# Kernel optimization log

Hardware: AMD Instinct MI355X
Metric: run time of the kernel (lower is better)

Reference implementation:

```python
import jax, jax.numpy as jnp
import numpy as np

D_MODEL = 256; N_HEADS = 8; N_LEVELS = 4; N_POINTS = 4; D_FFN = 1024
BS = 8; NQ = 100; NKPT = 17
LEVEL_SHAPES = [(160, 160), (80, 80), (40, 40), (20, 20)]  # (H, W) per level
LEN_V = sum(h * w for h, w in LEVEL_SHAPES)  # 34000


def layer_norm(x, g, b, eps=1e-5):
    m = x.mean(-1, keepdims=True)
    v = ((x - m) ** 2).mean(-1, keepdims=True)
    return (x - m) * jax.lax.rsqrt(v + eps) * g + b


def mha(q, k, v, Wqkv, bqkv, Wo, bo):
    # torch nn.MultiheadAttention, batch_first, eval mode (no dropout)
    d = q.shape[-1]; dh = d // N_HEADS
    def proj(x, W, b):
        return (x @ W.T + b).reshape(*x.shape[:-1], N_HEADS, dh)
    qp = proj(q, Wqkv[:d], bqkv[:d])
    kp = proj(k, Wqkv[d:2 * d], bqkv[d:2 * d])
    vp = proj(v, Wqkv[2 * d:], bqkv[2 * d:])
    att = jnp.einsum('bqhd,bkhd->bhqk', qp, kp) / jnp.sqrt(jnp.asarray(dh, q.dtype))
    att = jax.nn.softmax(att, -1)
    out = jnp.einsum('bhqk,bkhd->bqhd', att, vp).reshape(q.shape)
    return out @ Wo.T + bo


def bilinear_sample(val, loc, h, w):
    # val: (B, H, h*w, Dh); loc: (B, Lq, H, P, 2) normalized to [0,1]
    # matches F.grid_sample(align_corners=False, padding_mode='zeros') on grid 2*loc-1
    B, Lq, H, P, _ = loc.shape
    px = loc[..., 0] * w - 0.5
    py = loc[..., 1] * h - 0.5
    x0f = jnp.floor(px); y0f = jnp.floor(py)
    lx = px - x0f; ly = py - y0f
    x0 = x0f.astype(jnp.int32); y0 = y0f.astype(jnp.int32)
    out = jnp.zeros((B, H, Lq, P, val.shape[-1]), val.dtype)
    for dx, dy, wt in ((0, 0, (1 - lx) * (1 - ly)), (1, 0, lx * (1 - ly)),
                       (0, 1, (1 - lx) * ly), (1, 1, lx * ly)):
        xi = x0 + dx; yi = y0 + dy
        valid = ((xi >= 0) & (xi < w) & (yi >= 0) & (yi < h)).astype(val.dtype)
        idx = jnp.clip(yi, 0, h - 1) * w + jnp.clip(xi, 0, w - 1)  # (B,Lq,H,P)
        idx = idx.transpose(0, 2, 1, 3).reshape(B, H, Lq * P)
        g = jnp.take_along_axis(val, idx[..., None], axis=2).reshape(B, H, Lq, P, -1)
        out = out + g * (wt * valid).transpose(0, 2, 1, 3)[..., None]
    return out  # (B, H, Lq, P, Dh)


def ms_deform_attn(query, ref_points, memory, off_W, off_b, aw_W, aw_b,
                   val_W, val_b, outp_W, outp_b):
    B, Lq, _ = query.shape
    dh = D_MODEL // N_HEADS
    value = (memory @ val_W.T + val_b).reshape(B, LEN_V, N_HEADS, dh)
    off = (query @ off_W.T + off_b).reshape(B, Lq, N_HEADS, N_LEVELS, N_POINTS, 2)
    aw = (query @ aw_W.T + aw_b).reshape(B, Lq, N_HEADS, N_LEVELS * N_POINTS)
    aw = jax.nn.softmax(aw, -1).reshape(B, Lq, N_HEADS, N_LEVELS, N_POINTS)
    normalizer = jnp.array([[w, h] for h, w in LEVEL_SHAPES], dtype=query.dtype)  # (L,2) as (W,H)
    loc = ref_points[:, :, None, :, None, :] + off / normalizer[None, None, None, :, None, :]
    out = jnp.zeros((B, Lq, N_HEADS, dh), query.dtype)
    start = 0
    for l, (h, w) in enumerate(LEVEL_SHAPES):
        vl = value[:, start:start + h * w].transpose(0, 2, 1, 3)  # (B,H,hw,Dh)
        s = bilinear_sample(vl, loc[:, :, :, l], h, w)            # (B,H,Lq,P,Dh)
        out = out + jnp.einsum('bhqpd,bqhp->bqhd', s, aw[:, :, :, l])
        start += h * w
    return out.reshape(B, Lq, D_MODEL) @ outp_W.T + outp_b


def setup_inputs() -> dict:
    key = jax.random.key(0)
    ks = iter(jax.random.split(key, 40))
    d = D_MODEL
    def w(shape, s=0.02):
        return jax.random.normal(next(ks), shape, jnp.float32) * s
    inp = {
        'tgt_pose': jax.random.normal(next(ks), (BS, NQ, NKPT, d), jnp.float32),
        'tgt_pose_query_pos': jax.random.normal(next(ks), (BS, NQ, NKPT, d), jnp.float32),
        'tgt_pose_reference_points': jax.random.uniform(next(ks), (BS, NQ * NKPT, N_LEVELS, 2), jnp.float32),
        'memory': jax.random.normal(next(ks), (BS, LEN_V, d), jnp.float32),
        'win_Wqkv': w((3 * d, d)), 'win_bqkv': jnp.zeros((3 * d,), jnp.float32),
        'win_Wo': w((d, d)), 'win_bo': jnp.zeros((d,), jnp.float32),
        'win_ng': jnp.ones((d,), jnp.float32), 'win_nb': jnp.zeros((d,), jnp.float32),
        'acr_Wqkv': w((3 * d, d)), 'acr_bqkv': jnp.zeros((3 * d,), jnp.float32),
        'acr_Wo': w((d, d)), 'acr_bo': jnp.zeros((d,), jnp.float32),
        'acr_ng': jnp.ones((d,), jnp.float32), 'acr_nb': jnp.zeros((d,), jnp.float32),
        'off_W': w((N_HEADS * N_LEVELS * N_POINTS * 2, d)),
        'off_b': jax.random.uniform(next(ks), (N_HEADS * N_LEVELS * N_POINTS * 2,), jnp.float32, -1.0, 1.0),
        'aw_W': w((N_HEADS * N_LEVELS * N_POINTS, d)), 'aw_b': jnp.zeros((N_HEADS * N_LEVELS * N_POINTS,), jnp.float32),
        'val_W': w((d, d)), 'val_b': jnp.zeros((d,), jnp.float32),
        'outp_W': w((d, d)), 'outp_b': jnp.zeros((d,), jnp.float32),
        'gate_W': w((2 * d, 2 * d)), 'gate_b': jnp.zeros((2 * d,), jnp.float32),
        'gate_ng': jnp.ones((d,), jnp.float32), 'gate_nb': jnp.zeros((d,), jnp.float32),
        'ffn_W1': w((D_FFN, d)), 'ffn_b1': jnp.zeros((D_FFN,), jnp.float32),
        'ffn_W2': w((d, D_FFN)), 'ffn_b2': jnp.zeros((d,), jnp.float32),
        'n2_g': jnp.ones((d,), jnp.float32), 'n2_b': jnp.zeros((d,), jnp.float32),
        'memory_spatial_shapes': jnp.array(LEVEL_SHAPES, jnp.int32),
    }
    return inp


def reference(tgt_pose, tgt_pose_query_pos, tgt_pose_reference_points, memory,
              win_Wqkv, win_bqkv, win_Wo, win_bo, win_ng, win_nb,
              acr_Wqkv, acr_bqkv, acr_Wo, acr_bo, acr_ng, acr_nb,
              off_W, off_b, aw_W, aw_b, val_W, val_b, outp_W, outp_b,
              gate_W, gate_b, gate_ng, gate_nb,
              ffn_W1, ffn_b1, ffn_W2, ffn_b2, n2_g, n2_b,
              memory_spatial_shapes):
    bs, nq, K, d = tgt_pose.shape
    # with_pos_embed mutates tgt_pose in place in the torch code -> residual includes pos
    tgt = tgt_pose + tgt_pose_query_pos
    # within-attention over keypoints of each query
    x = tgt.reshape(bs * nq, K, d)
    t2 = mha(x, x, x, win_Wqkv, win_bqkv, win_Wo, win_bo).reshape(bs, nq, K, d)
    tgt = layer_norm(tgt + t2, win_ng, win_nb)
    # across-attention over queries for each keypoint
    xk = tgt.transpose(0, 2, 1, 3).reshape(bs * K, nq, d)
    t2 = mha(xk, xk, xk, acr_Wqkv, acr_bqkv, acr_Wo, acr_bo)
    tgt = layer_norm(xk + t2, acr_ng, acr_nb).reshape(bs, K, nq, d).transpose(0, 2, 1, 3)
    # second in-place pos add before deformable cross-attn (also feeds gateway)
    tgt_q = tgt + tgt_pose_query_pos
    t2 = ms_deform_attn(tgt_q.reshape(bs, nq * K, d), tgt_pose_reference_points, memory,
                        off_W, off_b, aw_W, aw_b, val_W, val_b, outp_W, outp_b)
    t2 = t2.reshape(bs, nq, K, d)
    # Gate
    g = jax.nn.sigmoid(jnp.concatenate([tgt_q, t2], -1) @ gate_W.T + gate_b)
    g1, g2 = jnp.split(g, 2, -1)
    tgt = layer_norm(g1 * tgt_q + g2 * t2, gate_ng, gate_nb)
    # FFN
    h = jax.nn.relu(tgt @ ffn_W1.T + ffn_b1)
    tgt = tgt + h @ ffn_W2.T + ffn_b2
    tgt = layer_norm(jnp.clip(tgt, -65504.0, 65504.0), n2_g, n2_b)
    return tgt
```

## Files before the change

### kernel.cpp

```cpp
#include <hip/hip_runtime.h>
#include <hip/hip_bf16.h>

#define NH 8
#define BS_ 8
#define NQ_ 100
#define NK_ 17
#define LQ 1700
#define T_TOK 13600
#define LEN_VV 34000

typedef __attribute__((ext_vector_type(8))) short short8v;
typedef __attribute__((ext_vector_type(8))) __bf16 bf16x8;
typedef __attribute__((ext_vector_type(4))) float f32x4;

__device__ __forceinline__ float wave_sum(float v){
#pragma unroll
  for (int m = 32; m; m >>= 1) v += __shfl_xor(v, m, 64);
  return v;
}
__device__ __forceinline__ short f2bf(float f){
  __hip_bfloat16 h = __float2bfloat16(f);
  return *reinterpret_cast<short*>(&h);
}
__device__ __forceinline__ float bf2f(short s){
  return __uint_as_float(((uint)(unsigned short)s) << 16);
}

__global__ __launch_bounds__(256) void add_k(const float* __restrict__ a,
                                             const float* __restrict__ b,
                                             float* __restrict__ o, int n4){
  int i = blockIdx.x * 256 + threadIdx.x;
  if (i >= n4) return;
  float4 x = ((const float4*)a)[i];
  float4 y = ((const float4*)b)[i];
  float4 r; r.x = x.x + y.x; r.y = x.y + y.y; r.z = x.z + y.z; r.w = x.w + y.w;
  ((float4*)o)[i] = r;
}

template<int EPI, int OUTB>
__global__ __launch_bounds__(256) void mgemm_k(const float* __restrict__ A,
                                               const float* __restrict__ W,
                                               const float* __restrict__ bias,
                                               float* __restrict__ Cf,
                                               __hip_bfloat16* __restrict__ Cb,
                                               int M, int N, int K){
  __shared__ short sh[OUTB ? 128 * 136 : 128 * 128];
  short* As = sh;
  short* Ws = sh + 128 * 64;
  const int tid = threadIdx.x;
  const int bm = blockIdx.y * 128, bn = blockIdx.x * 128;
  const int wave = tid >> 6, lane = tid & 63;
  const int wm = (wave >> 1) * 64, wn = (wave & 1) * 64;
  const int s = tid & 7;
  const int row0 = tid >> 3;
  f32x4 acc[4][4] = {};
  const int lrow = lane & 15, lk = lane >> 4;

  float4 ra[8], rw[8];
#pragma unroll
  for (int i = 0; i < 4; i++){
    int row = row0 + i * 32;
    int gr = bm + row;
    float4 z = make_float4(0.f, 0.f, 0.f, 0.f);
    if (gr < M){
      const float* p = A + (size_t)gr * K + s * 8;
      ra[2 * i] = ((const float4*)p)[0]; ra[2 * i + 1] = ((const float4*)p)[1];
    } else { ra[2 * i] = z; ra[2 * i + 1] = z; }
    const float* q = W + (size_t)(bn + row) * K + s * 8;
    rw[2 * i] = ((const float4*)q)[0]; rw[2 * i + 1] = ((const float4*)q)[1];
  }

  for (int k0 = 0; k0 < K; k0 += 64){
#pragma unroll
    for (int i = 0; i < 4; i++){
      int row = row0 + i * 32;
      int sw = ((s ^ (row & 7)) << 3) + row * 64;
      float4 a0 = ra[2 * i], a1 = ra[2 * i + 1];
      short8v v;
      v[0]=f2bf(a0.x); v[1]=f2bf(a0.y); v[2]=f2bf(a0.z); v[3]=f2bf(a0.w);
      v[4]=f2bf(a1.x); v[5]=f2bf(a1.y); v[6]=f2bf(a1.z); v[7]=f2bf(a1.w);
      *(short8v*)&As[sw] = v;
      a0 = rw[2 * i]; a1 = rw[2 * i + 1];
      short8v u;
      u[0]=f2bf(a0.x); u[1]=f2bf(a0.y); u[2]=f2bf(a0.z); u[3]=f2bf(a0.w);
      u[4]=f2bf(a1.x); u[5]=f2bf(a1.y); u[6]=f2bf(a1.z); u[7]=f2bf(a1.w);
      *(short8v*)&Ws[sw] = u;
    }
    __syncthreads();
    if (k0 + 64 < K){
#pragma unroll
      for (int i = 0; i < 4; i++){
        int row = row0 + i * 32;
        int gr = bm + row;
        float4 z = make_float4(0.f, 0.f, 0.f, 0.f);
        if (gr < M){
          const float* p = A + (size_t)gr * K + k0 + 64 + s * 8;
          ra[2 * i] = ((const float4*)p)[0]; ra[2 * i + 1] = ((const float4*)p)[1];
        } else { ra[2 * i] = z; ra[2 * i + 1] = z; }
        const float* q = W + (size_t)(bn + row) * K + k0 + 64 + s * 8;
        rw[2 * i] = ((const float4*)q)[0]; rw[2 * i + 1] = ((const float4*)q)[1];
      }
    }
#pragma unroll
    for (int ks = 0; ks < 2; ks++){
      short8v af[4], bw[4];
      int slot = ks * 4 + lk;
#pragma unroll
      for (int m = 0; m < 4; m++){
        int r = wm + m * 16 + lrow;
        af[m] = *(const short8v*)&As[r * 64 + ((slot ^ (r & 7)) << 3)];
      }
#pragma unroll
      for (int n = 0; n < 4; n++){
        int r = wn + n * 16 + lrow;
        bw[n] = *(const short8v*)&Ws[r * 64 + ((slot ^ (r & 7)) << 3)];
      }
#pragma unroll
      for (int m = 0; m < 4; m++)
#pragma unroll
        for (int n = 0; n < 4; n++)
          acc[m][n] = __builtin_amdgcn_mfma_f32_16x16x32_bf16(
              __builtin_bit_cast(bf16x8, af[m]),
              __builtin_bit_cast(bf16x8, bw[n]), acc[m][n], 0, 0, 0);
    }
    __syncthreads();
  }
  if (OUTB){
    const int STR = 136;
#pragma unroll
    for (int n = 0; n < 4; n++){
      int col = wn + n * 16 + lrow;
      float bsv = bias[bn + col];
#pragma unroll
      for (int m = 0; m < 4; m++){
#pragma unroll
        for (int i = 0; i < 4; i++){
          int row = wm + m * 16 + lk * 4 + i;
          float c = acc[m][n][i] + bsv;
          if (EPI == 1) c = fmaxf(c, 0.f);
          if (EPI == 2) c = 1.f / (1.f + expf(-c));
          sh[row * STR + col] = f2bf(c);
        }
      }
    }
    __syncthreads();
#pragma unroll
    for (int it = 0; it < 8; it++){
      int r = it * 16 + (tid >> 4);
      int chunk = tid & 15;
      if (bm + r < M){
        uint4 v = *(const uint4*)((const char*)sh + r * 272 + chunk * 16);
        *(uint4*)((char*)Cb + ((size_t)(bm + r) * N + bn) * 2 + chunk * 16) = v;
      }
    }
  } else {
#pragma unroll
    for (int n = 0; n < 4; n++){
      int col = bn + wn + n * 16 + lrow;
      float bsv = bias[col];
#pragma unroll
      for (int m = 0; m < 4; m++){
#pragma unroll
        for (int i = 0; i < 4; i++){
          int row = bm + wm + m * 16 + lk * 4 + i;
          if (row >= M) continue;
          float c = acc[m][n][i] + bsv;
          if (EPI == 1) c = fmaxf(c, 0.f);
          if (EPI == 2) c = 1.f / (1.f + expf(-c));
          Cf[(size_t)row * N + col] = c;
        }
      }
    }
  }
}

template<int EPI, int OUTB, int INB, int DUALA>
__global__ __launch_bounds__(256) void g64_k(const void* __restrict__ Av,
                                             const void* __restrict__ A1v,
                                             const float* __restrict__ W0,
                                             const float* __restrict__ W1,
                                             int NSPLIT,
                                             const float* __restrict__ bias0,
                                             const float* __restrict__ bias1,
                                             float* __restrict__ Cf,
                                             __hip_bfloat16* __restrict__ Cb,
                                             int M, int N, int K, int sA){
  __shared__ short sh64[2 * 64 * 64];
  short* As = sh64;
  short* Ws = sh64 + 64 * 64;
  const int tid = threadIdx.x;
  const int bn = blockIdx.x * 64, bm = blockIdx.y * 64;
  const int wave = tid >> 6, lane = tid & 63;
  const int wm = (wave >> 1) * 32, wn = (wave & 1) * 32;
  const int s = tid & 7, row0 = tid >> 3;
  const int lrow = lane & 15, lk = lane >> 4;
  f32x4 acc[2][2] = {};

  for (int k0 = 0; k0 < K; k0 += 64){
#pragma unroll
    for (int i = 0; i < 2; i++){
      int row = row0 + i * 32;
      int sw = ((s ^ (row & 7)) << 3) + row * 64;
      short8v v = {};
      int gr = bm + row;
      if (gr < M){
        if (INB){
          v = *(const short8v*)((const short*)Av + (size_t)gr * sA + k0 + s * 8);
        } else {
          const float* Ap;
          if (DUALA) Ap = (k0 < 256) ? (const float*)Av + (size_t)gr * 256 + k0
                                     : (const float*)A1v + (size_t)gr * 256 + (k0 - 256);
          else Ap = (const float*)Av + (size_t)gr * sA + k0;
          float4 a0 = ((const float4*)(Ap + s * 8))[0];
          float4 a1 = ((const float4*)(Ap + s * 8))[1];
          v[0]=f2bf(a0.x); v[1]=f2bf(a0.y); v[2]=f2bf(a0.z); v[3]=f2bf(a0.w);
          v[4]=f2bf(a1.x); v[5]=f2bf(a1.y); v[6]=f2bf(a1.z); v[7]=f2bf(a1.w);
        }
      }
      *(short8v*)&As[sw] = v;
      int wr = bn + row;
      const float* Wp = (wr < NSPLIT) ? W0 + (size_t)wr * K + k0
                                      : W1 + (size_t)(wr - NSPLIT) * K + k0;
      float4 b0 = ((const float4*)(Wp + s * 8))[0];
      float4 b1 = ((const float4*)(Wp + s * 8))[1];
      short8v u;
      u[0]=f2bf(b0.x); u[1]=f2bf(b0.y); u[2]=f2bf(b0.z); u[3]=f2bf(b0.w);
      u[4]=f2bf(b1.x); u[5]=f2bf(b1.y); u[6]=f2bf(b1.z); u[7]=f2bf(b1.w);
      *(short8v*)&Ws[sw] = u;
    }
    __syncthreads();
#pragma unroll
    for (int ks = 0; ks < 2; ks++){
      int slot = ks * 4 + lk;
      short8v af[2], bw[2];
#pragma unroll
      for (int m = 0; m < 2; m++){
        int r = wm + m * 16 + lrow;
        af[m] = *(const short8v*)&As[r * 64 + ((slot ^ (r & 7)) << 3)];
      }
#pragma unroll
      for (int n = 0; n < 2; n++){
        int r = wn + n * 16 + lrow;
        bw[n] = *(const short8v*)&Ws[r * 64 + ((slot ^ (r & 7)) << 3)];
      }
#pragma unroll
      for (int m = 0; m < 2; m++)
#pragma unroll
        for (int n = 0; n < 2; n++)
          acc[m][n] = __builtin_amdgcn_mfma_f32_16x16x32_bf16(
              __builtin_bit_cast(bf16x8, af[m]),
              __builtin_bit_cast(bf16x8, bw[n]), acc[m][n], 0, 0, 0);
    }
    __syncthreads();
  }
  if (OUTB){
    const int STR = 72;
#pragma unroll
    for (int n = 0; n < 2; n++){
      int col = wn + n * 16 + lrow;
      int gc = bn + col;
      float bsv = (gc < NSPLIT) ? bias0[gc] : bias1[gc - NSPLIT];
#pragma unroll
      for (int m = 0; m < 2; m++){
#pragma unroll
        for (int i = 0; i < 4; i++){
          int row = wm + m * 16 + lk * 4 + i;
          float c = acc[m][n][i] + bsv;
          if (EPI == 1) c = fmaxf(c, 0.f);
          if (EPI == 2) c = 1.f / (1.f + expf(-c));
          sh64[row * STR + col] = f2bf(c);
        }
      }
    }
    __syncthreads();
#pragma unroll
    for (int it = 0; it < 2; it++){
      int r = it * 32 + (tid >> 3);
      int chunk = tid & 7;
      if (bm + r < M){
        uint4 v = *(const uint4*)((const char*)sh64 + r * 144 + chunk * 16);
        *(uint4*)((char*)Cb + ((size_t)(bm + r) * N + bn) * 2 + chunk * 16) = v;
      }
    }
  } else {
#pragma unroll
    for (int n = 0; n < 2; n++){
      int gc = bn + wn + n * 16 + lrow;
      float bsv = (gc < NSPLIT) ? bias0[gc] : bias1[gc - NSPLIT];
#pragma unroll
      for (int m = 0; m < 2; m++){
#pragma unroll
        for (int i = 0; i < 4; i++){
          int row = bm + wm + m * 16 + lk * 4 + i;
          if (row >= M) continue;
          float c = acc[m][n][i] + bsv;
          if (EPI == 1) c = fmaxf(c, 0.f);
          if (EPI == 2) c = 1.f / (1.f + expf(-c));
          Cf[(size_t)row * N + gc] = c;
        }
      }
    }
  }
}

template<int TP>
__global__ __launch_bounds__(256) void mha_mfma_k(const short* __restrict__ qkv,
                                                  __hip_bfloat16* __restrict__ out, int S){
  constexpr int MT = TP / 16;
  constexpr int KSTEPS = (TP + 31) / 32;
  constexpr int KS32 = KSTEPS * 32;
  constexpr int VSTRB = (KS32 == 128) ? 256 : 128;
  __shared__ short QK[2][TP][64];
  __shared__ short Vt[2][32][VSTRB / 2];
  __shared__ float Sc[2][16][128];
  __shared__ float rinv[2][16];

  const int tid = threadIdx.x;
  const int bid = blockIdx.x;
  const int batch = bid >> 2, hp = bid & 3;
  const int wave = tid >> 6, lane = tid & 63;
  const int hh = wave >> 1, wsub = wave & 1;
  const int lrow = lane & 15, lk = lane >> 4;
  const float scale = 0.17677669529663687f;
  const size_t qbase = (size_t)batch * S * 768;

  for (int idx = tid; idx < 2 * TP * 4; idx += 256){
    int h2 = idx >= TP * 4;
    int rem = idx - h2 * TP * 4;
    int j = rem >> 2, s = rem & 3;
    int h = hp * 2 + h2;
    short8v qv = {}, kv = {};
    if (j < S){
      const short* p = qkv + qbase + (size_t)j * 768 + h * 32 + s * 8;
      qv = *(const short8v*)p;
      kv = *(const short8v*)(p + 256);
    }
    *(short8v*)&QK[h2][j][(s ^ (j & 7)) << 3] = qv;
    *(short8v*)&QK[h2][j][((s + 4) ^ (j & 7)) << 3] = kv;
  }
  for (int idx = tid; idx < 2 * KS32 * 4; idx += 256){
    int h2 = idx >= KS32 * 4;
    int rem = idx - h2 * KS32 * 4;
    int j = rem >> 2, e8 = rem & 3;
    int h = hp * 2 + h2;
    short8v v = {};
    if (j < S) v = *(const short8v*)(qkv + qbase + (size_t)j * 768 + h * 32 + 512 + e8 * 8);
#pragma unroll
    for (int c = 0; c < 8; c++){
      int e = e8 * 8 + c;
      char* pb = (char*)&Vt[h2][0][0] + e * VSTRB + (((j >> 3) ^ (e & 7)) << 4) + ((j & 7) << 1);
      *(short*)pb = v[c];
    }
  }
  __syncthreads();

  for (int mt = 0; mt < MT; mt++){
    for (int nt = wsub; nt < MT; nt += 2){
      int ar = mt * 16 + lrow;
      short8v aq = *(const short8v*)&QK[hh][ar][(lk ^ (ar & 7)) << 3];
      int br = nt * 16 + lrow;
      short8v bk = *(const short8v*)&QK[hh][br][((lk + 4) ^ (br & 7)) << 3];
      f32x4 z = {};
      f32x4 d = __builtin_amdgcn_mfma_f32_16x16x32_bf16(
          __builtin_bit_cast(bf16x8, aq), __builtin_bit_cast(bf16x8, bk), z, 0, 0, 0);
#pragma unroll
      for (int i = 0; i < 4; i++){
        int rr = lk * 4 + i;
        int c = nt * 16 + lrow;
        Sc[hh][rr][(((c >> 2) ^ (rr & 7)) << 2) + (c & 3)] = d[i] * scale;
      }
    }
    __syncthreads();
    if (wsub == 0){
      int rr = lane >> 2, p = lane & 3;
      int grow = mt * 16 + rr;
      int Seff = (grow < S) ? S : 0;
      float mx = -1e30f;
#pragma unroll
      for (int m = 0; m < KSTEPS; m++){
        int j = p + 4 * m;
#pragma unroll
        for (int half = 0; half < 2; half++){
          int ls = 2 * j + half;
          float4 v = *(const float4*)&Sc[hh][rr][(ls ^ (rr & 7)) << 2];
          int c0 = ls * 4;
          mx = fmaxf(mx, (c0 + 0 < Seff) ? v.x : -1e30f);
          mx = fmaxf(mx, (c0 + 1 < Seff) ? v.y : -1e30f);
          mx = fmaxf(mx, (c0 + 2 < Seff) ? v.z : -1e30f);
          mx = fmaxf(mx, (c0 + 3 < Seff) ? v.w : -1e30f);
        }
      }
      mx = fmaxf(mx, __shfl_xor(mx, 1, 64));
      mx = fmaxf(mx, __shfl_xor(mx, 2, 64));
      float sum = 0.f;
#pragma unroll
      for (int m = 0; m < KSTEPS; m++){
        int j = p + 4 * m;
        float ev[8];
#pragma unroll
        for (int half = 0; half < 2; half++){
          int ls = 2 * j + half;
          float4 v = *(const float4*)&Sc[hh][rr][(ls ^ (rr & 7)) << 2];
          int c0 = ls * 4;
          ev[half * 4 + 0] = (c0 + 0 < Seff) ? __expf(v.x - mx) : 0.f;
          ev[half * 4 + 1] = (c0 + 1 < Seff) ? __expf(v.y - mx) : 0.f;
          ev[half * 4 + 2] = (c0 + 2 < Seff) ? __expf(v.z - mx) : 0.f;
          ev[half * 4 + 3] = (c0 + 3 < Seff) ? __expf(v.w - mx) : 0.f;
        }
        short8v pb;
#pragma unroll
        for (int q2 = 0; q2 < 8; q2++){ pb[q2] = f2bf(ev[q2]); sum += ev[q2]; }
        *(short8v*)((char*)&Sc[hh][rr][0] + ((j ^ (rr & 7)) << 4)) = pb;
      }
      sum += __shfl_xor(sum, 1, 64);
      sum += __shfl_xor(sum, 2, 64);
      if (p == 0) rinv[hh][rr] = (sum > 0.f) ? 1.f / sum : 0.f;
    }
    __syncthreads();
    {
      int nt2 = wsub;
      f32x4 acc = {};
#pragma unroll
      for (int ks = 0; ks < KSTEPS; ks++){
        int slot = ks * 4 + lk;
        short8v ap = *(const short8v*)((const char*)&Sc[hh][lrow][0] + ((slot ^ (lrow & 7)) << 4));
        int e = nt2 * 16 + lrow;
        short8v bv = *(const short8v*)((const char*)&Vt[hh][0][0] + e * VSTRB + ((slot ^ (e & 7)) << 4));
        acc = __builtin_amdgcn_mfma_f32_16x16x32_bf16(
            __builtin_bit_cast(bf16x8, ap), __builtin_bit_cast(bf16x8, bv), acc, 0, 0, 0);
      }
      int h = hp * 2 + hh;
#pragma unroll
      for (int i = 0; i < 4; i++){
        int row = mt * 16 + lk * 4 + i;
        if (row < S){
          float rv = rinv[hh][lk * 4 + i];
          out[((size_t)batch * S + row) * 256 + h * 32 + nt2 * 16 + lrow] =
              __float2bfloat16(acc[i] * rv);
        }
      }
    }
    __syncthreads();
  }
}

template<int MODE>
__global__ __launch_bounds__(64) void ln_k(const float* __restrict__ a,
                                           const float* __restrict__ b,
                                           const float* __restrict__ g,
                                           const float* __restrict__ be,
                                           float* __restrict__ out,
                                           const float* __restrict__ qp){
  int r = blockIdx.x;
  int lane = threadIdx.x;
  float4 xa = *(const float4*)(a + (size_t)r * 256 + lane * 4);
  float4 xb = *(const float4*)(b + (size_t)r * 256 + lane * 4);
  float x[4] = { xa.x + xb.x, xa.y + xb.y, xa.z + xb.z, xa.w + xb.w };
  if (MODE == 2){
#pragma unroll
    for (int i = 0; i < 4; i++) x[i] = fminf(fmaxf(x[i], -65504.f), 65504.f);
  }
  float s = x[0] + x[1] + x[2] + x[3];
  s = wave_sum(s);
  float mean = s * (1.f / 256.f);
  float sq = 0.f;
#pragma unroll
  for (int i = 0; i < 4; i++){ float d = x[i] - mean; sq += d * d; }
  float var = wave_sum(sq) * (1.f / 256.f);
  float rstd = rsqrtf(var + 1e-5f);
  float4 gg = *(const float4*)(g + lane * 4);
  float4 bb = *(const float4*)(be + lane * 4);
  size_t orow = r;
  if (MODE == 3){
    int bi = r / LQ; int rem = r % LQ; int kk = rem / NQ_; int q = rem % NQ_;
    orow = (size_t)bi * LQ + q * NK_ + kk;
  }
  if (MODE == 4){
    int bi = r / LQ; int rem = r % LQ; int q = rem / NK_; int kk = rem % NK_;
    orow = (size_t)bi * LQ + kk * NQ_ + q;
  }
  float4 o;
  o.x = (x[0] - mean) * rstd * gg.x + bb.x;
  o.y = (x[1] - mean) * rstd * gg.y + bb.y;
  o.z = (x[2] - mean) * rstd * gg.z + bb.z;
  o.w = (x[3] - mean) * rstd * gg.w + bb.w;
  if (MODE == 3){
    float4 qv = *(const float4*)(qp + orow * 256 + lane * 4);
    o.x += qv.x; o.y += qv.y; o.z += qv.z; o.w += qv.w;
  }
  *(float4*)(out + orow * 256 + lane * 4) = o;
}

__global__ __launch_bounds__(64) void gate_ln_k(const short* __restrict__ G,
                                                const float* __restrict__ aq,
                                                const float* __restrict__ t2,
                                                const float* __restrict__ g,
                                                const float* __restrict__ be,
                                                float* __restrict__ out){
  int r = blockIdx.x;
  int lane = threadIdx.x;
  const short* gp = G + (size_t)r * 512 + lane * 4;
  float g1v[4], g2v[4];
#pragma unroll
  for (int i = 0; i < 4; i++){ g1v[i] = bf2f(gp[i]); g2v[i] = bf2f(gp[256 + i]); }
  float4 xa = *(const float4*)(aq + (size_t)r * 256 + lane * 4);
  float4 xt = *(const float4*)(t2 + (size_t)r * 256 + lane * 4);
  float x[4] = { g1v[0] * xa.x + g2v[0] * xt.x, g1v[1] * xa.y + g2v[1] * xt.y,
                 g1v[2] * xa.z + g2v[2] * xt.z, g1v[3] * xa.w + g2v[3] * xt.w };
  float s = x[0] + x[1] + x[2] + x[3];
  s = wave_sum(s);
  float mean = s * (1.f / 256.f);
  float sq = 0.f;
#pragma unroll
  for (int i = 0; i < 4; i++){ float d = x[i] - mean; sq += d * d; }
  float var = wave_sum(sq) * (1.f / 256.f);
  float rstd = rsqrtf(var + 1e-5f);
  float4 gg = *(const float4*)(g + lane * 4);
  float4 bb = *(const float4*)(be + lane * 4);
  float4 o;
  o.x = (x[0] - mean) * rstd * gg.x + bb.x;
  o.y = (x[1] - mean) * rstd * gg.y + bb.y;
  o.z = (x[2] - mean) * rstd * gg.z + bb.z;
  o.w = (x[3] - mean) * rstd * gg.w + bb.w;
  *(float4*)(out + (size_t)r * 256 + lane * 4) = o;
}

__global__ __launch_bounds__(256) void deform_k(const __hip_bfloat16* __restrict__ val,
                                                const float* __restrict__ offaw,
                                                const float* __restrict__ ref,
                                                unsigned int* __restrict__ outb){
  __shared__ uint2 meta[32][16][4];
  const int tid = threadIdx.x;
  const int t0 = blockIdx.x * 4;
  {
    int g = tid >> 3;
    int pair = tid & 7;
    int lt = g >> 3, h = g & 7;
    int t = t0 + lt;
    int b = t / LQ;
    int p0 = pair * 2;
    int l = p0 >> 2;
    const int starts[4] = {0, 25600, 32000, 33600};
    const int HS[4] = {160, 80, 40, 20};
    int w = HS[l];
    const float* ap = offaw + (size_t)t * 384 + 256 + h * 16;
    float a0 = ap[p0];
    float a1 = ap[p0 + 1];
    float mx = fmaxf(a0, a1);
#pragma unroll
    for (int m = 1; m <= 4; m <<= 1) mx = fmaxf(mx, __shfl_xor(mx, m, 64));
    float e0 = expf(a0 - mx), e1 = expf(a1 - mx);
    float s = e0 + e1;
#pragma unroll
    for (int m = 1; m <= 4; m <<= 1) s += __shfl_xor(s, m, 64);
    float inv = 1.f / s;
    float rx = ref[((size_t)t * 4 + l) * 2 + 0];
    float ry = ref[((size_t)t * 4 + l) * 2 + 1];
    float4 ov = *(const float4*)(offaw + (size_t)t * 384 + h * 32 + l * 8 + p0 * 2);
    int vbase = (b * LEN_VV + starts[l]) * 128 + h * 16;
#pragma unroll
    for (int pp = 0; pp < 2; pp++){
      float wgt = (pp ? e1 : e0) * inv;
      float px = rx * w + (pp ? ov.z : ov.x) - 0.5f;
      float py = ry * w + (pp ? ov.w : ov.y) - 0.5f;
      float x0f = floorf(px), y0f = floorf(py);
      float lx = px - x0f, ly = py - y0f;
      int x0 = (int)x0f, y0 = (int)y0f;
#pragma unroll
      for (int c = 0; c < 4; c++){
        int dx = c & 1, dy = c >> 1;
        int xi = x0 + dx, yi = y0 + dy;
        bool ok = (xi >= 0) & (xi < w) & (yi >= 0) & (yi < w);
        float cw = ok ? wgt * (dx ? lx : 1.f - lx) * (dy ? ly : 1.f - ly) : 0.f;
        uint idx = ok ? (uint)(vbase + (yi * w + xi) * 128) : 0u;
        uint2 m2; m2.x = idx; m2.y = __float_as_uint(cw);
        meta[g][p0 + pp][c] = m2;
      }
    }
  }
  __syncthreads();
  const uint* V2 = (const uint*)val;
  int sg = tid >> 4, lane = tid & 15;
#pragma unroll
  for (int it = 0; it < 2; it++){
    int g = it * 16 + sg;
    int lt = g >> 3, h = g & 7;
    int t = t0 + lt;
    float ax = 0.f, ay = 0.f;
#pragma unroll 4
    for (int c = 0; c < 64; c++){
      uint2 mw = meta[g][c >> 2][c & 3];
      float wv = __uint_as_float(mw.y);
      uint v = V2[(size_t)mw.x + lane];
      float lo = __uint_as_float(v << 16);
      float hi = __uint_as_float(v & 0xffff0000u);
      ax += wv * lo;
      ay += wv * hi;
    }
    uint u = ((uint)(unsigned short)f2bf(ay) << 16) | (uint)(unsigned short)f2bf(ax);
    outb[((size_t)t * 256 + h * 32) / 2 + lane] = u;
  }
}

extern "C" void kernel_launch(void* const* d_in, const int* in_sizes, int n_in,
                              void* d_out, int out_size, void* d_ws, size_t ws_size,
                              hipStream_t stream){
  const float* tgt_pose = (const float*)d_in[0];
  const float* qpos     = (const float*)d_in[1];
  const float* refp     = (const float*)d_in[2];
  const float* memory   = (const float*)d_in[3];
  const float* win_Wqkv = (const float*)d_in[4];
  const float* win_bqkv = (const float*)d_in[5];
  const float* win_Wo   = (const float*)d_in[6];
  const float* win_bo   = (const float*)d_in[7];
  const float* win_ng   = (const float*)d_in[8];
  const float* win_nb   = (const float*)d_in[9];
  const float* acr_Wqkv = (const float*)d_in[10];
  const float* acr_bqkv = (const float*)d_in[11];
  const float* acr_Wo   = (const float*)d_in[12];
  const float* acr_bo   = (const float*)d_in[13];
  const float* acr_ng   = (const float*)d_in[14];
  const float* acr_nb   = (const float*)d_in[15];
  const float* off_W    = (const float*)d_in[16];
  const float* off_b    = (const float*)d_in[17];
  const float* aw_W     = (const float*)d_in[18];
  const float* aw_b     = (const float*)d_in[19];
  const float* val_W    = (const float*)d_in[20];
  const float* val_b    = (const float*)d_in[21];
  const float* outp_W   = (const float*)d_in[22];
  const float* outp_b   = (const float*)d_in[23];
  const float* gate_W   = (const float*)d_in[24];
  const float* gate_b   = (const float*)d_in[25];
  const float* gate_ng  = (const float*)d_in[26];
  const float* gate_nb  = (const float*)d_in[27];
  const float* ffn_W1   = (const float*)d_in[28];
  const float* ffn_b1   = (const float*)d_in[29];
  const float* ffn_W2   = (const float*)d_in[30];
  const float* ffn_b2   = (const float*)d_in[31];
  const float* n2_g     = (const float*)d_in[32];
  const float* n2_b     = (const float*)d_in[33];

  float* out = (float*)d_out;
  char* ws = (char*)d_ws;
  const size_t TB = (size_t)T_TOK * 256 * 4;
  float* B0 = (float*)(ws);
  float* B1 = (float*)(ws + TB);
  float* B2 = (float*)(ws + 2 * TB);
  float* B3 = (float*)(ws + 3 * TB);
  char* p = ws + 4 * TB;
  short* Qb = (short*)p;                 p += (size_t)T_TOK * 768 * 2;
  short* ABF = (short*)p;                p += (size_t)T_TOK * 256 * 2;
  float* OFFAW = (float*)p;              p += (size_t)T_TOK * 384 * 4;
  short* Gb = (short*)p;                 p += (size_t)T_TOK * 512 * 2;
  char* Vregion = p;
  __hip_bfloat16* V = (__hip_bfloat16*)Vregion;
  short* FF = (short*)Vregion;

  const int n4 = T_TOK * 64;
  const int GM128 = (T_TOK + 127) / 128;
  const int GM64  = (T_TOK + 63) / 64;
  const int BIG = 1 << 30;

  add_k<<<(n4 + 255) / 256, 256, 0, stream>>>(tgt_pose, qpos, B0, n4);
  mgemm_k<0,1><<<dim3(6, GM128), 256, 0, stream>>>(B0, win_Wqkv, win_bqkv, nullptr, (__hip_bfloat16*)Qb, T_TOK, 768, 256);
  mha_mfma_k<32><<<800 * 4, 256, 0, stream>>>(Qb, (__hip_bfloat16*)ABF, 17);
  g64_k<0,0,1,0><<<dim3(4, GM64), 256, 0, stream>>>(ABF, nullptr, win_Wo, win_Wo, BIG, win_bo, win_bo, B2, nullptr, T_TOK, 256, 256, 256);
  ln_k<4><<<T_TOK, 64, 0, stream>>>(B0, B2, win_ng, win_nb, B1, nullptr);
  mgemm_k<0,1><<<dim3(6, GM128), 256, 0, stream>>>(B1, acr_Wqkv, acr_bqkv, nullptr, (__hip_bfloat16*)Qb, T_TOK, 768, 256);
  mha_mfma_k<112><<<136 * 4, 256, 0, stream>>>(Qb, (__hip_bfloat16*)ABF, 100);
  g64_k<0,0,1,0><<<dim3(4, GM64), 256, 0, stream>>>(ABF, nullptr, acr_Wo, acr_Wo, BIG, acr_bo, acr_bo, B2, nullptr, T_TOK, 256, 256, 256);
  ln_k<3><<<T_TOK, 64, 0, stream>>>(B1, B2, acr_ng, acr_nb, B0, qpos);
  mgemm_k<0,1><<<dim3(2, 2125), 256, 0, stream>>>(memory, val_W, val_b, nullptr, V, BS_ * LEN_VV, 256, 256);
  g64_k<0,0,0,0><<<dim3(6, GM64), 256, 0, stream>>>(B0, nullptr, off_W, aw_W, 256, off_b, aw_b, OFFAW, nullptr, T_TOK, 384, 256, 256);
  deform_k<<<T_TOK / 4, 256, 0, stream>>>(V, OFFAW, refp, (unsigned int*)ABF);
  g64_k<0,0,1,0><<<dim3(4, GM64), 256, 0, stream>>>(ABF, nullptr, outp_W, outp_W, BIG, outp_b, outp_b, B3, nullptr, T_TOK, 256, 256, 256);
  g64_k<2,1,0,1><<<dim3(8, GM64), 256, 0, stream>>>(B0, B3, gate_W, gate_W, BIG, gate_b, gate_b, nullptr, (__hip_bfloat16*)Gb, T_TOK, 512, 512, 256);
  gate_ln_k<<<T_TOK, 64, 0, stream>>>(Gb, B0, B3, gate_ng, gate_nb, B2);
  mgemm_k<1,1><<<dim3(8, GM128), 256, 0, stream>>>(B2, ffn_W1, ffn_b1, nullptr, (__hip_bfloat16*)FF, T_TOK, 1024, 256);
  g64_k<0,0,1,0><<<dim3(4, GM64), 256, 0, stream>>>(FF, nullptr, ffn_W2, ffn_W2, BIG, ffn_b2, ffn_b2, B1, nullptr, T_TOK, 256, 1024, 1024);
  ln_k<2><<<T_TOK, 64, 0, stream>>>(B2, B1, n2_g, n2_b, out, nullptr);
}
```

Measured before the change: 465.4 us.

## Fuse pos-add into QKV GEMM, split MHA blocks, swizzle value GEMM grid

Removes the standalone add kernel by summing tgt and query_pos inside the QKV GEMM loads, and re-adds query_pos in the layernorm instead. Folds the FFN residual into the second FFN GEMM epilogue so the final layernorm reads one tensor. Splits the across-query attention over two blocks per head pair for more parallelism. Also remaps the value-projection GEMM grid to a 1D layout with an XCD-aware swizzle and launches it first. The cost is more loads inside the GEMM and duplicated Q/K/V staging in the split attention blocks.

Result: no change. 472.6 us (+1.6%).

```diff
diff --git a/kernel.cpp b/kernel.cpp
--- a/kernel.cpp
+++ b/kernel.cpp
@@ -26,29 +26,27 @@
   return __uint_as_float(((uint)(unsigned short)s) << 16);
 }
 
-__global__ __launch_bounds__(256) void add_k(const float* __restrict__ a,
-                                             const float* __restrict__ b,
-                                             float* __restrict__ o, int n4){
-  int i = blockIdx.x * 256 + threadIdx.x;
-  if (i >= n4) return;
-  float4 x = ((const float4*)a)[i];
-  float4 y = ((const float4*)b)[i];
-  float4 r; r.x = x.x + y.x; r.y = x.y + y.y; r.z = x.z + y.z; r.w = x.w + y.w;
-  ((float4*)o)[i] = r;
-}
-
-template<int EPI, int OUTB>
+template<int EPI, int ADDA, int SWZ>
 __global__ __launch_bounds__(256) void mgemm_k(const float* __restrict__ A,
+                                               const float* __restrict__ A2,
                                                const float* __restrict__ W,
                                                const float* __restrict__ bias,
-                                               float* __restrict__ Cf,
                                                __hip_bfloat16* __restrict__ Cb,
-                                               int M, int N, int K){
-  __shared__ short sh[OUTB ? 128 * 136 : 128 * 128];
+                                               int M, int N, int K, int nbx){
+  __shared__ short sh[128 * 136];
   short* As = sh;
   short* Ws = sh + 128 * 64;
+  int j;
+  if (SWZ){
+    int total = gridDim.x;
+    int q = total >> 3, r = total & 7;
+    int x = blockIdx.x & 7, k = blockIdx.x >> 3;
+    j = (x < r) ? x * (q + 1) + k : r * (q + 1) + (x - r) * q + k;
+  } else {
+    j = blockIdx.x;
+  }
   const int tid = threadIdx.x;
-  const int bm = blockIdx.y * 128, bn = blockIdx.x * 128;
+  const int bm = (j / nbx) * 128, bn = (j % nbx) * 128;
   const int wave = tid >> 6, lane = tid & 63;
   const int wm = (wave >> 1) * 64, wn = (wave & 1) * 64;
   const int s = tid & 7;
@@ -64,7 +62,14 @@
     float4 z = make_float4(0.f, 0.f, 0.f, 0.f);
     if (gr < M){
       const float* p = A + (size_t)gr * K + s * 8;
-      ra[2 * i] = ((const float4*)p)[0]; ra[2 * i + 1] = ((const float4*)p)[1];
+      float4 x0 = ((const float4*)p)[0], x1 = ((const float4*)p)[1];
+      if (ADDA){
+        const float* q2 = A2 + (size_t)gr * K + s * 8;
+        float4 y0 = ((const float4*)q2)[0], y1 = ((const float4*)q2)[1];
+        x0.x+=y0.x; x0.y+=y0.y; x0.z+=y0.z; x0.w+=y0.w;
+        x1.x+=y1.x; x1.y+=y1.y; x1.z+=y1.z; x1.w+=y1.w;
+      }
+      ra[2 * i] = x0; ra[2 * i + 1] = x1;
     } else { ra[2 * i] = z; ra[2 * i + 1] = z; }
     const float* q = W + (size_t)(bn + row) * K + s * 8;
     rw[2 * i] = ((const float4*)q)[0]; rw[2 * i + 1] = ((const float4*)q)[1];
@@ -95,7 +100,14 @@
         float4 z = make_float4(0.f, 0.f, 0.f, 0.f);
         if (gr < M){
           const float* p = A + (size_t)gr * K + k0 + 64 + s * 8;
-          ra[2 * i] = ((const float4*)p)[0]; ra[2 * i + 1] = ((const float4*)p)[1];
+          float4 x0 = ((const float4*)p)[0], x1 = ((const float4*)p)[1];
+          if (ADDA){
+            const float* q2 = A2 + (size_t)gr * K + k0 + 64 + s * 8;
+            float4 y0 = ((const float4*)q2)[0], y1 = ((const float4*)q2)[1];
+            x0.x+=y0.x; x0.y+=y0.y; x0.z+=y0.z; x0.w+=y0.w;
+            x1.x+=y1.x; x1.y+=y1.y; x1.z+=y1.z; x1.w+=y1.w;
+          }
+          ra[2 * i] = x0; ra[2 * i + 1] = x1;
         } else { ra[2 * i] = z; ra[2 * i + 1] = z; }
         const float* q = W + (size_t)(bn + row) * K + k0 + 64 + s * 8;
         rw[2 * i] = ((const float4*)q)[0]; rw[2 * i + 1] = ((const float4*)q)[1];
@@ -125,51 +137,30 @@
     }
     __syncthreads();
   }
-  if (OUTB){
-    const int STR = 136;
-#pragma unroll
-    for (int n = 0; n < 4; n++){
-      int col = wn + n * 16 + lrow;
-      float bsv = bias[bn + col];
-#pragma unroll
-      for (int m = 0; m < 4; m++){
-#pragma unroll
-        for (int i = 0; i < 4; i++){
-          int row = wm + m * 16 + lk * 4 + i;
-          float c = acc[m][n][i] + bsv;
-          if (EPI == 1) c = fmaxf(c, 0.f);
-          if (EPI == 2) c = 1.f / (1.f + expf(-c));
-          sh[row * STR + col] = f2bf(c);
-        }
-      }
-    }
-    __syncthreads();
-#pragma unroll
-    for (int it = 0; it < 8; it++){
-      int r = it * 16 + (tid >> 4);
-      int chunk = tid & 15;
-      if (bm + r < M){
-        uint4 v = *(const uint4*)((const char*)sh + r * 272 + chunk * 16);
-        *(uint4*)((char*)Cb + ((size_t)(bm + r) * N + bn) * 2 + chunk * 16) = v;
-      }
-    }
-  } else {
-#pragma unroll
-    for (int n = 0; n < 4; n++){
-      int col = bn + wn + n * 16 + lrow;
-      float bsv = bias[col];
-#pragma unroll
-      for (int m = 0; m < 4; m++){
-#pragma unroll
-        for (int i = 0; i < 4; i++){
-          int row = bm + wm + m * 16 + lk * 4 + i;
-          if (row >= M) continue;
-          float c = acc[m][n][i] + bsv;
-          if (EPI == 1) c = fmaxf(c, 0.f);
-          if (EPI == 2) c = 1.f / (1.f + expf(-c));
-          Cf[(size_t)row * N + col] = c;
-        }
-      }
+  const int STR = 136;
+#pragma unroll
+  for (int n = 0; n < 4; n++){
+    int col = wn + n * 16 + lrow;
+    float bsv = bias[bn + col];
+#pragma unroll
+    for (int m = 0; m < 4; m++){
+#pragma unroll
+      for (int i = 0; i < 4; i++){
+        int row = wm + m * 16 + lk * 4 + i;
+        float c = acc[m][n][i] + bsv;
+        if (EPI == 1) c = fmaxf(c, 0.f);
+        sh[row * STR + col] = f2bf(c);
+      }
+    }
+  }
+  __syncthreads();
+#pragma unroll
+  for (int it = 0; it < 8; it++){
+    int r = it * 16 + (tid >> 4);
+    int chunk = tid & 15;
+    if (bm + r < M){
+      uint4 v = *(const uint4*)((const char*)sh + r * 272 + chunk * 16);
+      *(uint4*)((char*)Cb + ((size_t)(bm + r) * N + bn) * 2 + chunk * 16) = v;
     }
   }
 }
@@ -182,6 +173,7 @@
                                              int NSPLIT,
                                              const float* __restrict__ bias0,
                                              const float* __restrict__ bias1,
+                                             const float* __restrict__ RES,
                                              float* __restrict__ Cf,
                                              __hip_bfloat16* __restrict__ Cb,
                                              int M, int N, int K, int sA){
@@ -296,6 +288,7 @@
           float c = acc[m][n][i] + bsv;
           if (EPI == 1) c = fmaxf(c, 0.f);
           if (EPI == 2) c = 1.f / (1.f + expf(-c));
+          if (EPI == 3) c += RES[(size_t)row * N + gc];
           Cf[(size_t)row * N + gc] = c;
         }
       }
@@ -303,13 +296,14 @@
   }
 }
 
-template<int TP>
+template<int TP, int NSPL>
 __global__ __launch_bounds__(256) void mha_mfma_k(const short* __restrict__ qkv,
                                                   __hip_bfloat16* __restrict__ out, int S){
   constexpr int MT = TP / 16;
   constexpr int KSTEPS = (TP + 31) / 32;
   constexpr int KS32 = KSTEPS * 32;
   constexpr int VSTRB = (KS32 == 128) ? 256 : 128;
+  constexpr int CH = (MT + NSPL - 1) / NSPL;
   __shared__ short QK[2][TP][64];
   __shared__ short Vt[2][32][VSTRB / 2];
   __shared__ float Sc[2][16][128];
@@ -317,7 +311,12 @@
 
   const int tid = threadIdx.x;
   const int bid = blockIdx.x;
-  const int batch = bid >> 2, hp = bid & 3;
+  const int batch = bid / (4 * NSPL);
+  const int rem = bid % (4 * NSPL);
+  const int hp = rem / NSPL;
+  const int half = rem % NSPL;
+  const int mtlo = half * CH;
+  const int mthi = (mtlo + CH < MT) ? (mtlo + CH) : MT;
   const int wave = tid >> 6, lane = tid & 63;
   const int hh = wave >> 1, wsub = wave & 1;
   const int lrow = lane & 15, lk = lane >> 4;
@@ -326,8 +325,8 @@
 
   for (int idx = tid; idx < 2 * TP * 4; idx += 256){
     int h2 = idx >= TP * 4;
-    int rem = idx - h2 * TP * 4;
-    int j = rem >> 2, s = rem & 3;
+    int rm = idx - h2 * TP * 4;
+    int j = rm >> 2, s = rm & 3;
     int h = hp * 2 + h2;
     short8v qv = {}, kv = {};
     if (j < S){
@@ -340,8 +339,8 @@
   }
   for (int idx = tid; idx < 2 * KS32 * 4; idx += 256){
     int h2 = idx >= KS32 * 4;
-    int rem = idx - h2 * KS32 * 4;
-    int j = rem >> 2, e8 = rem & 3;
+    int rm = idx - h2 * KS32 * 4;
+    int j = rm >> 2, e8 = rm & 3;
     int h = hp * 2 + h2;
     short8v v = {};
     if (j < S) v = *(const short8v*)(qkv + qbase + (size_t)j * 768 + h * 32 + 512 + e8 * 8);
@@ -354,7 +353,7 @@
   }
   __syncthreads();
 
-  for (int mt = 0; mt < MT; mt++){
+  for (int mt = mtlo; mt < mthi; mt++){
     for (int nt = wsub; nt < MT; nt += 2){
       int ar = mt * 16 + lrow;
       short8v aq = *(const short8v*)&QK[hh][ar][(lk ^ (ar & 7)) << 3];
@@ -380,8 +379,8 @@
       for (int m = 0; m < KSTEPS; m++){
         int j = p + 4 * m;
 #pragma unroll
-        for (int half = 0; half < 2; half++){
-          int ls = 2 * j + half;
+        for (int hf = 0; hf < 2; hf++){
+          int ls = 2 * j + hf;
           float4 v = *(const float4*)&Sc[hh][rr][(ls ^ (rr & 7)) << 2];
           int c0 = ls * 4;
           mx = fmaxf(mx, (c0 + 0 < Seff) ? v.x : -1e30f);
@@ -398,14 +397,14 @@
         int j = p + 4 * m;
         float ev[8];
 #pragma unroll
-        for (int half = 0; half < 2; half++){
-          int ls = 2 * j + half;
+        for (int hf = 0; hf < 2; hf++){
+          int ls = 2 * j + hf;
           float4 v = *(const float4*)&Sc[hh][rr][(ls ^ (rr & 7)) << 2];
           int c0 = ls * 4;
-          ev[half * 4 + 0] = (c0 + 0 < Seff) ? __expf(v.x - mx) : 0.f;
-          ev[half * 4 + 1] = (c0 + 1 < Seff) ? __expf(v.y - mx) : 0.f;
-          ev[half * 4 + 2] = (c0 + 2 < Seff) ? __expf(v.z - mx) : 0.f;
-          ev[half * 4 + 3] = (c0 + 3 < Seff) ? __expf(v.w - mx) : 0.f;
+          ev[hf * 4 + 0] = (c0 + 0 < Seff) ? __expf(v.x - mx) : 0.f;
+          ev[hf * 4 + 1] = (c0 + 1 < Seff) ? __expf(v.y - mx) : 0.f;
+          ev[hf * 4 + 2] = (c0 + 2 < Seff) ? __expf(v.z - mx) : 0.f;
+          ev[hf * 4 + 3] = (c0 + 3 < Seff) ? __expf(v.w - mx) : 0.f;
         }
         short8v pb;
 #pragma unroll
@@ -450,13 +449,21 @@
                                            const float* __restrict__ g,
                                            const float* __restrict__ be,
                                            float* __restrict__ out,
-                                           const float* __restrict__ qp){
+                                           const float* __restrict__ qpre,
+                                           const float* __restrict__ qpost){
   int r = blockIdx.x;
   int lane = threadIdx.x;
   float4 xa = *(const float4*)(a + (size_t)r * 256 + lane * 4);
-  float4 xb = *(const float4*)(b + (size_t)r * 256 + lane * 4);
-  float x[4] = { xa.x + xb.x, xa.y + xb.y, xa.z + xb.z, xa.w + xb.w };
-  if (MODE == 2){
+  float x[4] = { xa.x, xa.y, xa.z, xa.w };
+  if (MODE != 5){
+    float4 xb = *(const float4*)(b + (size_t)r * 256 + lane * 4);
+    x[0] += xb.x; x[1] += xb.y; x[2] += xb.z; x[3] += xb.w;
+  }
+  if (MODE == 4){
+    float4 xq = *(const float4*)(qpre + (size_t)r * 256 + lane * 4);
+    x[0] += xq.x; x[1] += xq.y; x[2] += xq.z; x[3] += xq.w;
+  }
+  if (MODE == 5){
 #pragma unroll
     for (int i = 0; i < 4; i++) x[i] = fminf(fmaxf(x[i], -65504.f), 65504.f);
   }
@@ -485,7 +492,7 @@
   o.z = (x[2] - mean) * rstd * gg.z + bb.z;
   o.w = (x[3] - mean) * rstd * gg.w + bb.w;
   if (MODE == 3){
-    float4 qv = *(const float4*)(qp + orow * 256 + lane * 4);
+    float4 qv = *(const float4*)(qpost + orow * 256 + lane * 4);
     o.x += qv.x; o.y += qv.y; o.z += qv.z; o.w += qv.w;
   }
   *(float4*)(out + orow * 256 + lane * 4) = o;
@@ -567,7 +574,7 @@
       float lx = px - x0f, ly = py - y0f;
       int x0 = (int)x0f, y0 = (int)y0f;
 #pragma unroll
-      for (int c = 0; c < 4; c++){
+    for (int c = 0; c < 4; c++){
         int dx = c & 1, dy = c >> 1;
         int xi = x0 + dx, yi = y0 + dy;
         bool ok = (xi >= 0) & (xi < w) & (yi >= 0) & (yi < w);
@@ -656,27 +663,25 @@
   __hip_bfloat16* V = (__hip_bfloat16*)Vregion;
   short* FF = (short*)Vregion;
 
-  const int n4 = T_TOK * 64;
   const int GM128 = (T_TOK + 127) / 128;
   const int GM64  = (T_TOK + 63) / 64;
   const int BIG = 1 << 30;
 
-  add_k<<<(n4 + 255) / 256, 256, 0, stream>>>(tgt_pose, qpos, B0, n4);
-  mgemm_k<0,1><<<dim3(6, GM128), 256, 0, stream>>>(B0, win_Wqkv, win_bqkv, nullptr, (__hip_bfloat16*)Qb, T_TOK, 768, 256);
-  mha_mfma_k<32><<<800 * 4, 256, 0, stream>>>(Qb, (__hip_bfloat16*)ABF, 17);
-  g64_k<0,0,1,0><<<dim3(4, GM64), 256, 0, stream>>>(ABF, nullptr, win_Wo, win_Wo, BIG, win_bo, win_bo, B2, nullptr, T_TOK, 256, 256, 256);
-  ln_k<4><<<T_TOK, 64, 0, stream>>>(B0, B2, win_ng, win_nb, B1, nullptr);
-  mgemm_k<0,1><<<dim3(6, GM128), 256, 0, stream>>>(B1, acr_Wqkv, acr_bqkv, nullptr, (__hip_bfloat16*)Qb, T_TOK, 768, 256);
-  mha_mfma_k<112><<<136 * 4, 256, 0, stream>>>(Qb, (__hip_bfloat16*)ABF, 100);
-  g64_k<0,0,1,0><<<dim3(4, GM64), 256, 0, stream>>>(ABF, nullptr, acr_Wo, acr_Wo, BIG, acr_bo, acr_bo, B2, nullptr, T_TOK, 256, 256, 256);
-  ln_k<3><<<T_TOK, 64, 0, stream>>>(B1, B2, acr_ng, acr_nb, B0, qpos);
-  mgemm_k<0,1><<<dim3(2, 2125), 256, 0, stream>>>(memory, val_W, val_b, nullptr, V, BS_ * LEN_VV, 256, 256);
-  g64_k<0,0,0,0><<<dim3(6, GM64), 256, 0, stream>>>(B0, nullptr, off_W, aw_W, 256, off_b, aw_b, OFFAW, nullptr, T_TOK, 384, 256, 256);
+  mgemm_k<0,0,1><<<2 * 2125, 256, 0, stream>>>(memory, nullptr, val_W, val_b, V, BS_ * LEN_VV, 256, 256, 2);
+  mgemm_k<0,1,0><<<6 * GM128, 256, 0, stream>>>(tgt_pose, qpos, win_Wqkv, win_bqkv, (__hip_bfloat16*)Qb, T_TOK, 768, 256, 6);
+  mha_mfma_k<32,1><<<800 * 4, 256, 0, stream>>>(Qb, (__hip_bfloat16*)ABF, 17);
+  g64_k<0,0,1,0><<<dim3(4, GM64), 256, 0, stream>>>(ABF, nullptr, win_Wo, win_Wo, BIG, win_bo, win_bo, nullptr, B2, nullptr, T_TOK, 256, 256, 256);
+  ln_k<4><<<T_TOK, 64, 0, stream>>>(tgt_pose, B2, win_ng, win_nb, B1, qpos, nullptr);
+  mgemm_k<0,0,0><<<6 * GM128, 256, 0, stream>>>(B1, nullptr, acr_Wqkv, acr_bqkv, (__hip_bfloat16*)Qb, T_TOK, 768, 256, 6);
+  mha_mfma_k<112,2><<<136 * 8, 256, 0, stream>>>(Qb, (__hip_bfloat16*)ABF, 100);
+  g64_k<0,0,1,0><<<dim3(4, GM64), 256, 0, stream>>>(ABF, nullptr, acr_Wo, acr_Wo, BIG, acr_bo, acr_bo, nullptr, B2, nullptr, T_TOK, 256, 256, 256);
+  ln_k<3><<<T_TOK, 64, 0, stream>>>(B1, B2, acr_ng, acr_nb, B0, nullptr, qpos);
+  g64_k<0,0,0,0><<<dim3(6, GM64), 256, 0, stream>>>(B0, nullptr, off_W, aw_W, 256, off_b, aw_b, nullptr, OFFAW, nullptr, T_TOK, 384, 256, 256);
   deform_k<<<T_TOK / 4, 256, 0, stream>>>(V, OFFAW, refp, (unsigned int*)ABF);
-  g64_k<0,0,1,0><<<dim3(4, GM64), 256, 0, stream>>>(ABF, nullptr, outp_W, outp_W, BIG, outp_b, outp_b, B3, nullptr, T_TOK, 256, 256, 256);
-  g64_k<2,1,0,1><<<dim3(8, GM64), 256, 0, stream>>>(B0, B3, gate_W, gate_W, BIG, gate_b, gate_b, nullptr, (__hip_bfloat16*)Gb, T_TOK, 512, 512, 256);
+  g64_k<0,0,1,0><<<dim3(4, GM64), 256, 0, stream>>>(ABF, nullptr, outp_W, outp_W, BIG, outp_b, outp_b, nullptr, B3, nullptr, T_TOK, 256, 256, 256);
+  g64_k<2,1,0,1><<<dim3(8, GM64), 256, 0, stream>>>(B0, B3, gate_W, gate_W, BIG, gate_b, gate_b, nullptr, nullptr, (__hip_bfloat16*)Gb, T_TOK, 512, 512, 256);
   gate_ln_k<<<T_TOK, 64, 0, stream>>>(Gb, B0, B3, gate_ng, gate_nb, B2);
-  mgemm_k<1,1><<<dim3(8, GM128), 256, 0, stream>>>(B2, ffn_W1, ffn_b1, nullptr, (__hip_bfloat16*)FF, T_TOK, 1024, 256);
-  g64_k<0,0,1,0><<<dim3(4, GM64), 256, 0, stream>>>(FF, nullptr, ffn_W2, ffn_W2, BIG, ffn_b2, ffn_b2, B1, nullptr, T_TOK, 256, 1024, 1024);
-  ln_k<2><<<T_TOK, 64, 0, stream>>>(B2, B1, n2_g, n2_b, out, nullptr);
-}
+  mgemm_k<1,0,0><<<8 * GM128, 256, 0, stream>>>(B2, nullptr, ffn_W1, ffn_b1, (__hip_bfloat16*)FF, T_TOK, 1024, 256, 8);
+  g64_k<3,0,1,0><<<dim3(4, GM64), 256, 0, stream>>>(FF, nullptr, ffn_W2, ffn_W2, BIG, ffn_b2, ffn_b2, B2, B1, nullptr, T_TOK, 256, 1024, 1024);
+  ln_k<5><<<T_TOK, 64, 0, stream>>>(B1, nullptr, n2_g, n2_b, out, nullptr, nullptr);
+}
```
